# Kernel tuning notes

Measured on AMD Instinct MI355X. Metric: run time of the kernel, lower is better.

## Reference

```python
import jax, jax.numpy as jnp
import numpy as np

LEAK = 0.2          # LeakyReLU negative slope
NEG = -9e15         # mask fill value from the original module
N, FIN, FOUT = 8192, 256, 128


def setup_inputs() -> dict:
    key = jax.random.key(0)
    k1, k2, k3, k4 = jax.random.split(key, 4)
    x = jax.random.normal(k1, (N, FIN), dtype=jnp.float32)
    # dense 0/1 adjacency mask, p(edge) ~= 0.5
    adj = jax.random.randint(k2, (N, N), 0, 2, dtype=jnp.int32)
    # xavier_uniform with gain sqrt(2)
    gW = np.sqrt(2.0) * np.sqrt(6.0 / (FIN + FOUT))
    W = jax.random.uniform(k3, (FIN, FOUT), dtype=jnp.float32, minval=-gW, maxval=gW)
    ga = np.sqrt(2.0) * np.sqrt(6.0 / (FOUT + 1))
    a = jax.random.uniform(k4, (FOUT, 1), dtype=jnp.float32, minval=-ga, maxval=ga)
    return {"x": x, "adj": adj, "W": W, "a": a}


def reference(x, adj, W, a):
    # h = X W                                     [N, FOUT]
    h = x @ W
    # alpha_j = a . h_j  -- the original's h.repeat(N,1) @ a reduces to this,
    # since every row block of the repeat is identical.
    alpha = jnp.squeeze(h @ a, axis=-1)           # [N]
    e = jax.nn.leaky_relu(alpha, LEAK)            # [N]
    # e_ij depends only on column j; broadcast across rows, then mask.
    scores = jnp.where(adj > 0, e[None, :], NEG)  # [N, N]
    attention = jax.nn.softmax(scores, axis=1)    # [N, N]
    # dropout: eval mode (training=False) -> identity
    h_prime = attention @ h                       # [N, FOUT]
    return h_prime
```

## Files before the change

### kernel.cpp

```cpp
#include <hip/hip_runtime.h>
#include <hip/hip_bf16.h>

#define NN 8192
#define FIN 256
#define FOUT 128
#define KSPLIT 2
#define KHALF (NN / KSPLIT)

typedef __attribute__((ext_vector_type(8))) short short8;
typedef __attribute__((ext_vector_type(4))) float f32x4;
typedef unsigned short u16;

__device__ inline u16 bf16r(float v) {
  return __builtin_bit_cast(u16, __float2bfloat16(v));
}

__global__ __launch_bounds__(256) void k_prep(const float* __restrict__ x,
                                              const float* __restrict__ W,
                                              const float* __restrict__ a,
                                              float* __restrict__ wexp,
                                              u16* __restrict__ gT) {
  __shared__ float xs[32 * 256];
  __shared__ float ap[4][16];
  __shared__ float wsh[32];
  __shared__ u16 gsh[32][132];
  const int t = threadIdx.x;
  const int r0 = blockIdx.x * 32;

  const float4* xg = (const float4*)(x + (size_t)r0 * FIN);
  float4* xs4 = (float4*)xs;
#pragma unroll
  for (int p = 0; p < 8; ++p) xs4[p * 256 + t] = xg[p * 256 + t];
  __syncthreads();

  const int f = t & 127;
  const int half = t >> 7;
  float acc[16];
#pragma unroll
  for (int i = 0; i < 16; ++i) acc[i] = 0.f;

  const float4* xsr = (const float4*)(xs + half * 16 * 256);
  for (int k4 = 0; k4 < 64; ++k4) {
    float w0 = W[(k4 * 4 + 0) * FOUT + f];
    float w1 = W[(k4 * 4 + 1) * FOUT + f];
    float w2 = W[(k4 * 4 + 2) * FOUT + f];
    float w3 = W[(k4 * 4 + 3) * FOUT + f];
#pragma unroll
    for (int i = 0; i < 16; ++i) {
      float4 xv = xsr[i * 64 + k4];
      acc[i] = fmaf(xv.x, w0, acc[i]);
      acc[i] = fmaf(xv.y, w1, acc[i]);
      acc[i] = fmaf(xv.z, w2, acc[i]);
      acc[i] = fmaf(xv.w, w3, acc[i]);
    }
  }

  const float af = a[f];
  float part[16];
#pragma unroll
  for (int i = 0; i < 16; ++i) part[i] = acc[i] * af;
#pragma unroll
  for (int i = 0; i < 16; ++i) {
#pragma unroll
    for (int off = 32; off >= 1; off >>= 1) part[i] += __shfl_xor(part[i], off);
  }
  const int wvid = t >> 6;
  if ((t & 63) == 0) {
#pragma unroll
    for (int i = 0; i < 16; ++i) ap[wvid][i] = part[i];
  }
  __syncthreads();
  if (t < 32) {
    int i = t & 15, hh = t >> 4;
    float alpha = ap[hh * 2][i] + ap[hh * 2 + 1][i];
    float ee = alpha > 0.f ? alpha : 0.2f * alpha;
    float wv = __expf(fminf(ee, 80.f));
    wsh[t] = wv;
    wexp[r0 + t] = wv;
  }
  __syncthreads();

#pragma unroll
  for (int i = 0; i < 16; ++i) {
    int row = half * 16 + i;
    gsh[row][f] = bf16r(acc[i] * wsh[row]);
  }
  __syncthreads();

  const int ff = t >> 1;
  const int jc = (t & 1) * 16;
  u16* dst = gT + (size_t)ff * NN + r0 + jc;
#pragma unroll
  for (int q = 0; q < 4; ++q) {
    ushort4 v;
    v.x = gsh[jc + q * 4 + 0][ff];
    v.y = gsh[jc + q * 4 + 1][ff];
    v.z = gsh[jc + q * 4 + 2][ff];
    v.w = gsh[jc + q * 4 + 3][ff];
    *(ushort4*)(dst + q * 4) = v;
  }
}

__global__ __launch_bounds__(512, 4) void k_gemm(const int* __restrict__ adj,
                                                 const u16* __restrict__ gT,
                                                 const float* __restrict__ w,
                                                 float* __restrict__ numer,
                                                 float* __restrict__ denom) {
  __shared__ u16 Ash[2][32 * 64];
  __shared__ u16 Bsh[2][128 * 64];
  __shared__ float denom_sh[32];

  const int t = threadIdx.x;
  const int lane = t & 63;
  const int wvid = t >> 6;
  const int wr = wvid >> 2;
  const int wc = wvid & 3;
  const int r0 = blockIdx.x * 32;
  const int ks = blockIdx.y;
  const size_t kbase = (size_t)ks * KHALF;

  const int ar = t >> 4;
  const int ako = (t & 15) * 4;
  const int* adjrow = adj + (size_t)(r0 + ar) * NN + kbase + ako;
  const float* wp = w + kbase + ako;
  const int bfr = t >> 3;
  const int bck = (t & 7) * 8;
  const u16* gTb = gT + kbase + bck;

  f32x4 acc0 = {0.f, 0.f, 0.f, 0.f};
  f32x4 acc1 = {0.f, 0.f, 0.f, 0.f};
  float dpart = 0.f;

  int4 av;
  float4 wq;
  short8 bb0, bb1;

  auto LOAD = [&](int kt) {
    av = *(const int4*)(adjrow + kt * 64);
    wq = *(const float4*)(wp + kt * 64);
    const u16* gp = gTb + (size_t)bfr * NN + kt * 64;
    bb0 = *(const short8*)gp;
    bb1 = *(const short8*)(gp + (size_t)64 * NN);
  };
  auto STORE = [&](int buf) {
    dpart += (av.x ? wq.x : 0.f) + (av.y ? wq.y : 0.f) +
             (av.z ? wq.z : 0.f) + (av.w ? wq.w : 0.f);
    ushort4 a4;
    a4.x = av.x ? (u16)0x3F80 : (u16)0;
    a4.y = av.y ? (u16)0x3F80 : (u16)0;
    a4.z = av.z ? (u16)0x3F80 : (u16)0;
    a4.w = av.w ? (u16)0x3F80 : (u16)0;
    int abyte = ar * 128 + ((ako * 2) ^ ((ar & 7) << 4));
    *(ushort4*)((char*)&Ash[buf][0] + abyte) = a4;
    int bbyte = bfr * 128 + ((bck * 2) ^ ((bfr & 7) << 4));
    *(short8*)((char*)&Bsh[buf][0] + bbyte) = bb0;
    *(short8*)((char*)&Bsh[buf][0] + bbyte + 64 * 128) = bb1;
  };
  auto COMPUTE = [&](int buf) {
    const int swz = (lane & 7) << 4;
    const int arow = wr * 16 + (lane & 15);
    const int bcol = wc * 32 + (lane & 15);
#pragma unroll
    for (int kc = 0; kc < 2; ++kc) {
      int kbyte = kc * 64 + (lane >> 4) * 16;
      short8 afr = *(const short8*)((const char*)&Ash[buf][0] + arow * 128 + (kbyte ^ swz));
      short8 b0  = *(const short8*)((const char*)&Bsh[buf][0] + bcol * 128 + (kbyte ^ swz));
      short8 b1  = *(const short8*)((const char*)&Bsh[buf][0] + (bcol + 16) * 128 + (kbyte ^ swz));
      acc0 = __builtin_amdgcn_mfma_f32_16x16x32_bf16(afr, b0, acc0, 0, 0, 0);
      acc1 = __builtin_amdgcn_mfma_f32_16x16x32_bf16(afr, b1, acc1, 0, 0, 0);
    }
  };

  const int NT = KHALF / 64;
  LOAD(0);
  STORE(0);
  LOAD(1);
  __syncthreads();
  for (int kt = 0; kt < NT; ++kt) {
    int buf = kt & 1;
    if (kt + 1 < NT) STORE(buf ^ 1);
    if (kt + 2 < NT) LOAD(kt + 2);
    COMPUTE(buf);
    __syncthreads();
  }

  dpart += __shfl_xor(dpart, 1);
  dpart += __shfl_xor(dpart, 2);
  dpart += __shfl_xor(dpart, 4);
  dpart += __shfl_xor(dpart, 8);
  if ((t & 15) == 0) denom_sh[ar] = dpart;
  __syncthreads();

#pragma unroll
  for (int q = 0; q < 4; ++q) {
    int row = wr * 16 + (lane >> 4) * 4 + q;
    int col = wc * 32 + (lane & 15);
    float* np = numer + ((size_t)ks * NN + r0 + row) * FOUT + col;
    np[0] = acc0[q];
    np[16] = acc1[q];
  }
  if (t < 32) denom[(size_t)ks * NN + r0 + t] = denom_sh[t];
}

__global__ __launch_bounds__(256) void k_comb(const float* __restrict__ numer,
                                              const float* __restrict__ denom,
                                              float* __restrict__ out) {
  const int idx = blockIdx.x * 256 + threadIdx.x;
  const int row = idx >> 5;
  const int fc = (idx & 31) * 4;
  float4 n0 = *(const float4*)(numer + (size_t)row * FOUT + fc);
  float4 n1 = *(const float4*)(numer + (size_t)(NN + row) * FOUT + fc);
  float d = denom[row] + denom[NN + row];
  float inv = 1.0f / d;
  float4 o;
  o.x = (n0.x + n1.x) * inv;
  o.y = (n0.y + n1.y) * inv;
  o.z = (n0.z + n1.z) * inv;
  o.w = (n0.w + n1.w) * inv;
  *(float4*)(out + (size_t)row * FOUT + fc) = o;
}

extern "C" void kernel_launch(void* const* d_in, const int* in_sizes, int n_in,
                              void* d_out, int out_size, void* d_ws, size_t ws_size,
                              hipStream_t stream) {
  const float* x = (const float*)d_in[0];
  const int* adj = (const int*)d_in[1];
  const float* W = (const float*)d_in[2];
  const float* a = (const float*)d_in[3];
  float* out = (float*)d_out;

  char* ws = (char*)d_ws;
  float* wexp = (float*)ws;
  u16* gT = (u16*)(ws + 64 * 1024);
  float* numer = (float*)(ws + 4 * 1024 * 1024);
  float* denom = (float*)(ws + 12 * 1024 * 1024);

  hipLaunchKernelGGL(k_prep, dim3(NN / 32), dim3(256), 0, stream, x, W, a, wexp, gT);
  hipLaunchKernelGGL(k_gemm, dim3(NN / 32, KSPLIT), dim3(512), 0, stream, adj, gT, wexp,
                     numer, denom);
  hipLaunchKernelGGL(k_comb, dim3((NN * FOUT / 4) / 256), dim3(256), 0, stream, numer,
                     denom, out);
}
```

Measured before the change: 96.44 us.

## Deepen global prefetch to four register sets with manual barrier scheduling

Changes the k_gemm main loop from a distance-2 register prefetch to a rotating set of four register stages, so global loads run about four tiles ahead. LDS fragment reads are issued before a single barrier per iteration, with sched_barrier and explicit waitcnt, so MFMAs run after the barrier. The aim is to hide HBM latency on the adjacency and gT streams. The extra registers may lower occupancy, and the hand-placed waits and barriers put correctness at risk if the double-buffer reuse ordering is wrong.

```diff
diff --git a/kernel.cpp b/kernel.cpp
--- a/kernel.cpp
+++ b/kernel.cpp
@@ -125,64 +125,98 @@
   const float* wp = w + kbase + ako;
   const int bfr = t >> 3;
   const int bck = (t & 7) * 8;
-  const u16* gTb = gT + kbase + bck;
-
+  const u16* gTb = gT + kbase + (size_t)bfr * NN + bck;
+
+  struct Set {
+    int4 av;
+    float4 wq;
+    short8 bb0, bb1;
+  };
+  Set s0, s1, s2, s3;
   f32x4 acc0 = {0.f, 0.f, 0.f, 0.f};
   f32x4 acc1 = {0.f, 0.f, 0.f, 0.f};
   float dpart = 0.f;
 
-  int4 av;
-  float4 wq;
-  short8 bb0, bb1;
-
-  auto LOAD = [&](int kt) {
-    av = *(const int4*)(adjrow + kt * 64);
-    wq = *(const float4*)(wp + kt * 64);
-    const u16* gp = gTb + (size_t)bfr * NN + kt * 64;
-    bb0 = *(const short8*)gp;
-    bb1 = *(const short8*)(gp + (size_t)64 * NN);
-  };
-  auto STORE = [&](int buf) {
-    dpart += (av.x ? wq.x : 0.f) + (av.y ? wq.y : 0.f) +
-             (av.z ? wq.z : 0.f) + (av.w ? wq.w : 0.f);
+  const int abyte = ar * 128 + ((ako * 2) ^ ((ar & 7) << 4));
+  const int bbyte = bfr * 128 + ((bck * 2) ^ ((bfr & 7) << 4));
+  const int swz = (lane & 7) << 4;
+  const int arow = wr * 16 + (lane & 15);
+  const int bcol = wc * 32 + (lane & 15);
+  const int k0 = (lane >> 4) * 16;
+
+  auto LOAD = [&](Set& S, int T) {
+    S.av = *(const int4*)(adjrow + T * 64);
+    S.wq = *(const float4*)(wp + T * 64);
+    S.bb0 = *(const short8*)(gTb + T * 64);
+    S.bb1 = *(const short8*)(gTb + T * 64 + (size_t)64 * NN);
+  };
+  auto STORE = [&](Set& S, int buf) {
+    dpart += (S.av.x ? S.wq.x : 0.f) + (S.av.y ? S.wq.y : 0.f) +
+             (S.av.z ? S.wq.z : 0.f) + (S.av.w ? S.wq.w : 0.f);
     ushort4 a4;
-    a4.x = av.x ? (u16)0x3F80 : (u16)0;
-    a4.y = av.y ? (u16)0x3F80 : (u16)0;
-    a4.z = av.z ? (u16)0x3F80 : (u16)0;
-    a4.w = av.w ? (u16)0x3F80 : (u16)0;
-    int abyte = ar * 128 + ((ako * 2) ^ ((ar & 7) << 4));
+    a4.x = S.av.x ? (u16)0x3F80 : (u16)0;
+    a4.y = S.av.y ? (u16)0x3F80 : (u16)0;
+    a4.z = S.av.z ? (u16)0x3F80 : (u16)0;
+    a4.w = S.av.w ? (u16)0x3F80 : (u16)0;
     *(ushort4*)((char*)&Ash[buf][0] + abyte) = a4;
-    int bbyte = bfr * 128 + ((bck * 2) ^ ((bfr & 7) << 4));
-    *(short8*)((char*)&Bsh[buf][0] + bbyte) = bb0;
-    *(short8*)((char*)&Bsh[buf][0] + bbyte + 64 * 128) = bb1;
-  };
-  auto COMPUTE = [&](int buf) {
-    const int swz = (lane & 7) << 4;
-    const int arow = wr * 16 + (lane & 15);
-    const int bcol = wc * 32 + (lane & 15);
-#pragma unroll
-    for (int kc = 0; kc < 2; ++kc) {
-      int kbyte = kc * 64 + (lane >> 4) * 16;
-      short8 afr = *(const short8*)((const char*)&Ash[buf][0] + arow * 128 + (kbyte ^ swz));
-      short8 b0  = *(const short8*)((const char*)&Bsh[buf][0] + bcol * 128 + (kbyte ^ swz));
-      short8 b1  = *(const short8*)((const char*)&Bsh[buf][0] + (bcol + 16) * 128 + (kbyte ^ swz));
-      acc0 = __builtin_amdgcn_mfma_f32_16x16x32_bf16(afr, b0, acc0, 0, 0, 0);
-      acc1 = __builtin_amdgcn_mfma_f32_16x16x32_bf16(afr, b1, acc1, 0, 0, 0);
-    }
-  };
-
-  const int NT = KHALF / 64;
-  LOAD(0);
-  STORE(0);
-  LOAD(1);
-  __syncthreads();
-  for (int kt = 0; kt < NT; ++kt) {
-    int buf = kt & 1;
-    if (kt + 1 < NT) STORE(buf ^ 1);
-    if (kt + 2 < NT) LOAD(kt + 2);
-    COMPUTE(buf);
-    __syncthreads();
-  }
+    *(short8*)((char*)&Bsh[buf][0] + bbyte) = S.bb0;
+    *(short8*)((char*)&Bsh[buf][0] + bbyte + 64 * 128) = S.bb1;
+  };
+
+  short8 fa0, fb00, fb10, fa1, fb01, fb11;
+  auto READS = [&](int buf) {
+    const char* A = (const char*)&Ash[buf][0];
+    const char* B = (const char*)&Bsh[buf][0];
+    fa0 = *(const short8*)(A + arow * 128 + (k0 ^ swz));
+    fb00 = *(const short8*)(B + bcol * 128 + (k0 ^ swz));
+    fb10 = *(const short8*)(B + (bcol + 16) * 128 + (k0 ^ swz));
+    fa1 = *(const short8*)(A + arow * 128 + ((64 + k0) ^ swz));
+    fb01 = *(const short8*)(B + bcol * 128 + ((64 + k0) ^ swz));
+    fb11 = *(const short8*)(B + (bcol + 16) * 128 + ((64 + k0) ^ swz));
+  };
+  auto MFMAS = [&]() {
+    acc0 = __builtin_amdgcn_mfma_f32_16x16x32_bf16(fa0, fb00, acc0, 0, 0, 0);
+    acc1 = __builtin_amdgcn_mfma_f32_16x16x32_bf16(fa0, fb10, acc1, 0, 0, 0);
+    acc0 = __builtin_amdgcn_mfma_f32_16x16x32_bf16(fa1, fb01, acc0, 0, 0, 0);
+    acc1 = __builtin_amdgcn_mfma_f32_16x16x32_bf16(fa1, fb11, acc1, 0, 0, 0);
+  };
+
+#define BODY(J, SW, DOST, DOLD)                             \
+  do {                                                      \
+    if (DOST) STORE(SW, ((J) + 1) & 1);                     \
+    if (DOLD) LOAD(SW, (J) + 5);                            \
+    READS((J) & 1);                                         \
+    asm volatile("s_waitcnt lgkmcnt(0)" ::: "memory");      \
+    __builtin_amdgcn_s_barrier();                           \
+    __builtin_amdgcn_sched_barrier(0);                      \
+    MFMAS();                                                \
+  } while (0)
+
+  LOAD(s0, 0);
+  STORE(s0, 0);
+  LOAD(s1, 1);
+  LOAD(s2, 2);
+  LOAD(s3, 3);
+  LOAD(s0, 4);
+  asm volatile("s_waitcnt lgkmcnt(0)" ::: "memory");
+  __builtin_amdgcn_s_barrier();
+  __builtin_amdgcn_sched_barrier(0);
+
+  for (int jb = 0; jb < 56; jb += 4) {
+    BODY(jb + 0, s1, 1, 1);
+    BODY(jb + 1, s2, 1, 1);
+    BODY(jb + 2, s3, 1, 1);
+    BODY(jb + 3, s0, 1, 1);
+  }
+  BODY(56, s1, 1, 1);
+  BODY(57, s2, 1, 1);
+  BODY(58, s3, 1, 1);
+  BODY(59, s0, 1, 0);
+  BODY(60, s1, 1, 0);
+  BODY(61, s2, 1, 0);
+  BODY(62, s3, 1, 0);
+  BODY(63, s0, 0, 0);
+#undef BODY
 
   dpart += __shfl_xor(dpart, 1);
   dpart += __shfl_xor(dpart, 2);
```

Result: no change. 97.89 us (+1.5%).

## Replace LDS-staged GEMM with register-direct MFMA and split K four ways

Applied to the files above, without the earlier changes.

The adjacency-weighted GEMM no longer stages tiles in LDS. Each wave loads its adjacency fragment directly into MFMA operand layout with nontemporal loads, packs the 0/1 values into bf16 with an integer multiply, and reads gT B-fragments straight from global memory with double-buffered registers. K is split four ways instead of two, and the combine kernel sums four partials. This removes LDS stores, loads and block barriers. In exchange each wave rereads the full B panel from global/L2, uses more registers, and writes more partial output.

```diff
diff --git a/kernel.cpp b/kernel.cpp
--- a/kernel.cpp
+++ b/kernel.cpp
@@ -4,12 +4,16 @@
 #define NN 8192
 #define FIN 256
 #define FOUT 128
-#define KSPLIT 2
-#define KHALF (NN / KSPLIT)
+#define KSPLIT 4
+#define KCH (NN / KSPLIT)
+#define NT (KCH / 32)
 
 typedef __attribute__((ext_vector_type(8))) short short8;
 typedef __attribute__((ext_vector_type(4))) float f32x4;
+typedef __attribute__((ext_vector_type(4))) int i32x4;
+typedef __attribute__((ext_vector_type(4))) unsigned int u32x4;
 typedef unsigned short u16;
+typedef unsigned int u32;
 
 __device__ inline u16 bf16r(float v) {
   return __builtin_bit_cast(u16, __float2bfloat16(v));
@@ -101,105 +105,99 @@
   }
 }
 
-__global__ __launch_bounds__(512, 4) void k_gemm(const int* __restrict__ adj,
-                                                 const u16* __restrict__ gT,
-                                                 const float* __restrict__ w,
-                                                 float* __restrict__ numer,
-                                                 float* __restrict__ denom) {
-  __shared__ u16 Ash[2][32 * 64];
-  __shared__ u16 Bsh[2][128 * 64];
-  __shared__ float denom_sh[32];
-
+__global__ __launch_bounds__(256) void k_mm(const int* __restrict__ adj,
+                                            const u16* __restrict__ gT,
+                                            const float* __restrict__ wexp,
+                                            float* __restrict__ numer,
+                                            float* __restrict__ denom) {
   const int t = threadIdx.x;
   const int lane = t & 63;
-  const int wvid = t >> 6;
-  const int wr = wvid >> 2;
-  const int wc = wvid & 3;
-  const int r0 = blockIdx.x * 32;
+  const int wv = t >> 6;
+  const int i0 = blockIdx.x * 64 + wv * 16;
   const int ks = blockIdx.y;
-  const size_t kbase = (size_t)ks * KHALF;
-
-  const int ar = t >> 4;
-  const int ako = (t & 15) * 4;
-  const int* adjrow = adj + (size_t)(r0 + ar) * NN + kbase + ako;
-  const float* wp = w + kbase + ako;
-  const int bfr = t >> 3;
-  const int bck = (t & 7) * 8;
-  const u16* gTb = gT + kbase + bck;
-
-  f32x4 acc0 = {0.f, 0.f, 0.f, 0.f};
-  f32x4 acc1 = {0.f, 0.f, 0.f, 0.f};
+  const int kbase = ks * KCH;
+  const int r = lane & 15;
+  const int ksl = lane >> 4;
+
+  const int* ap = adj + (size_t)(i0 + r) * NN + kbase + ksl * 8;
+  const float* wp = wexp + kbase + ksl * 8;
+  const u16* gp = gT + (size_t)r * NN + kbase + ksl * 8;
+
+  f32x4 acc[8];
+#pragma unroll
+  for (int n = 0; n < 8; ++n) acc[n] = (f32x4){0.f, 0.f, 0.f, 0.f};
   float dpart = 0.f;
 
-  int4 av;
-  float4 wq;
-  short8 bb0, bb1;
-
-  auto LOAD = [&](int kt) {
-    av = *(const int4*)(adjrow + kt * 64);
-    wq = *(const float4*)(wp + kt * 64);
-    const u16* gp = gTb + (size_t)bfr * NN + kt * 64;
-    bb0 = *(const short8*)gp;
-    bb1 = *(const short8*)(gp + (size_t)64 * NN);
+  i32x4 avE0, avE1, avO0, avO1;
+  f32x4 wvE0, wvE1, wvO0, wvO1;
+  short8 fbE[8], fbO[8];
+
+  auto LDA = [&](int kt, i32x4& a0, i32x4& a1, f32x4& w0, f32x4& w1) {
+    const i32x4* p = (const i32x4*)(ap + kt * 32);
+    a0 = __builtin_nontemporal_load(p);
+    a1 = __builtin_nontemporal_load(p + 1);
+    const f32x4* q = (const f32x4*)(wp + kt * 32);
+    w0 = q[0];
+    w1 = q[1];
   };
-  auto STORE = [&](int buf) {
-    dpart += (av.x ? wq.x : 0.f) + (av.y ? wq.y : 0.f) +
-             (av.z ? wq.z : 0.f) + (av.w ? wq.w : 0.f);
-    ushort4 a4;
-    a4.x = av.x ? (u16)0x3F80 : (u16)0;
-    a4.y = av.y ? (u16)0x3F80 : (u16)0;
-    a4.z = av.z ? (u16)0x3F80 : (u16)0;
-    a4.w = av.w ? (u16)0x3F80 : (u16)0;
-    int abyte = ar * 128 + ((ako * 2) ^ ((ar & 7) << 4));
-    *(ushort4*)((char*)&Ash[buf][0] + abyte) = a4;
-    int bbyte = bfr * 128 + ((bck * 2) ^ ((bfr & 7) << 4));
-    *(short8*)((char*)&Bsh[buf][0] + bbyte) = bb0;
-    *(short8*)((char*)&Bsh[buf][0] + bbyte + 64 * 128) = bb1;
+  auto LDB = [&](int kt, short8* fb) {
+#pragma unroll
+    for (int n = 0; n < 8; ++n)
+      fb[n] = *(const short8*)(gp + (size_t)n * 16 * NN + kt * 32);
   };
-  auto COMPUTE = [&](int buf) {
-    const int swz = (lane & 7) << 4;
-    const int arow = wr * 16 + (lane & 15);
-    const int bcol = wc * 32 + (lane & 15);
-#pragma unroll
-    for (int kc = 0; kc < 2; ++kc) {
-      int kbyte = kc * 64 + (lane >> 4) * 16;
-      short8 afr = *(const short8*)((const char*)&Ash[buf][0] + arow * 128 + (kbyte ^ swz));
-      short8 b0  = *(const short8*)((const char*)&Bsh[buf][0] + bcol * 128 + (kbyte ^ swz));
-      short8 b1  = *(const short8*)((const char*)&Bsh[buf][0] + (bcol + 16) * 128 + (kbyte ^ swz));
-      acc0 = __builtin_amdgcn_mfma_f32_16x16x32_bf16(afr, b0, acc0, 0, 0, 0);
-      acc1 = __builtin_amdgcn_mfma_f32_16x16x32_bf16(afr, b1, acc1, 0, 0, 0);
+  auto STEP = [&](i32x4 a0, i32x4 a1, f32x4 w0, f32x4 w1, short8* fb) {
+    u32 p0 = ((u32)a0[0] + ((u32)a0[1] << 16)) * 0x3F80u;
+    u32 p1 = ((u32)a0[2] + ((u32)a0[3] << 16)) * 0x3F80u;
+    u32 p2 = ((u32)a1[0] + ((u32)a1[1] << 16)) * 0x3F80u;
+    u32 p3 = ((u32)a1[2] + ((u32)a1[3] << 16)) * 0x3F80u;
+    u32x4 pv = {p0, p1, p2, p3};
+    short8 fa = __builtin_bit_cast(short8, pv);
+    dpart += (a0[0] ? w0[0] : 0.f) + (a0[1] ? w0[1] : 0.f) +
+             (a0[2] ? w0[2] : 0.f) + (a0[3] ? w0[3] : 0.f) +
+             (a1[0] ? w1[0] : 0.f) + (a1[1] ? w1[1] : 0.f) +
+             (a1[2] ? w1[2] : 0.f) + (a1[3] ? w1[3] : 0.f);
+#pragma unroll
+    for (int n = 0; n < 8; ++n)
+      acc[n] = __builtin_amdgcn_mfma_f32_16x16x32_bf16(fa, fb[n], acc[n], 0, 0, 0);
+  };
+
+  LDA(0, avE0, avE1, wvE0, wvE1);
+  LDA(1, avO0, avO1, wvO0, wvO1);
+  LDB(0, fbE);
+
+#pragma unroll 1
+  for (int kt = 0; kt < NT; kt += 2) {
+    {
+      i32x4 a0 = avE0, a1 = avE1;
+      f32x4 w0 = wvE0, w1 = wvE1;
+      int ka = (kt + 2 < NT) ? kt + 2 : 0;
+      LDA(ka, avE0, avE1, wvE0, wvE1);
+      LDB(kt + 1, fbO);
+      STEP(a0, a1, w0, w1, fbE);
     }
-  };
-
-  const int NT = KHALF / 64;
-  LOAD(0);
-  STORE(0);
-  LOAD(1);
-  __syncthreads();
-  for (int kt = 0; kt < NT; ++kt) {
-    int buf = kt & 1;
-    if (kt + 1 < NT) STORE(buf ^ 1);
-    if (kt + 2 < NT) LOAD(kt + 2);
-    COMPUTE(buf);
-    __syncthreads();
-  }
-
-  dpart += __shfl_xor(dpart, 1);
-  dpart += __shfl_xor(dpart, 2);
-  dpart += __shfl_xor(dpart, 4);
-  dpart += __shfl_xor(dpart, 8);
-  if ((t & 15) == 0) denom_sh[ar] = dpart;
-  __syncthreads();
-
+    {
+      i32x4 a0 = avO0, a1 = avO1;
+      f32x4 w0 = wvO0, w1 = wvO1;
+      int ka = (kt + 3 < NT) ? kt + 3 : 0;
+      LDA(ka, avO0, avO1, wvO0, wvO1);
+      int kb = (kt + 2 < NT) ? kt + 2 : 0;
+      LDB(kb, fbE);
+      STEP(a0, a1, w0, w1, fbO);
+    }
+  }
+
+  dpart += __shfl_xor(dpart, 16);
+  dpart += __shfl_xor(dpart, 32);
+  if (lane < 16) denom[(size_t)ks * NN + i0 + lane] = dpart;
+
+  float* np = numer + ((size_t)ks * NN + i0) * FOUT;
 #pragma unroll
   for (int q = 0; q < 4; ++q) {
-    int row = wr * 16 + (lane >> 4) * 4 + q;
-    int col = wc * 32 + (lane & 15);
-    float* np = numer + ((size_t)ks * NN + r0 + row) * FOUT + col;
-    np[0] = acc0[q];
-    np[16] = acc1[q];
-  }
-  if (t < 32) denom[(size_t)ks * NN + r0 + t] = denom_sh[t];
+    int row = (lane >> 4) * 4 + q;
+#pragma unroll
+    for (int n = 0; n < 8; ++n)
+      np[(size_t)row * FOUT + n * 16 + (lane & 15)] = acc[n][q];
+  }
 }
 
 __global__ __launch_bounds__(256) void k_comb(const float* __restrict__ numer,
@@ -208,15 +206,23 @@
   const int idx = blockIdx.x * 256 + threadIdx.x;
   const int row = idx >> 5;
   const int fc = (idx & 31) * 4;
-  float4 n0 = *(const float4*)(numer + (size_t)row * FOUT + fc);
-  float4 n1 = *(const float4*)(numer + (size_t)(NN + row) * FOUT + fc);
-  float d = denom[row] + denom[NN + row];
+  float4 s = {0.f, 0.f, 0.f, 0.f};
+  float d = 0.f;
+#pragma unroll
+  for (int ks = 0; ks < KSPLIT; ++ks) {
+    float4 nv = *(const float4*)(numer + ((size_t)ks * NN + row) * FOUT + fc);
+    s.x += nv.x;
+    s.y += nv.y;
+    s.z += nv.z;
+    s.w += nv.w;
+    d += denom[(size_t)ks * NN + row];
+  }
   float inv = 1.0f / d;
   float4 o;
-  o.x = (n0.x + n1.x) * inv;
-  o.y = (n0.y + n1.y) * inv;
-  o.z = (n0.z + n1.z) * inv;
-  o.w = (n0.w + n1.w) * inv;
+  o.x = s.x * inv;
+  o.y = s.y * inv;
+  o.z = s.z * inv;
+  o.w = s.w * inv;
   *(float4*)(out + (size_t)row * FOUT + fc) = o;
 }
 
@@ -231,12 +237,12 @@
 
   char* ws = (char*)d_ws;
   float* wexp = (float*)ws;
-  u16* gT = (u16*)(ws + 64 * 1024);
-  float* numer = (float*)(ws + 4 * 1024 * 1024);
-  float* denom = (float*)(ws + 12 * 1024 * 1024);
+  u16* gT = (u16*)(ws + (size_t)65536);
+  float* numer = (float*)(ws + (size_t)65536 + 2097152);
+  float* denom = (float*)(ws + (size_t)65536 + 2097152 + 16777216);
 
   hipLaunchKernelGGL(k_prep, dim3(NN / 32), dim3(256), 0, stream, x, W, a, wexp, gT);
-  hipLaunchKernelGGL(k_gemm, dim3(NN / 32, KSPLIT), dim3(512), 0, stream, adj, gT, wexp,
+  hipLaunchKernelGGL(k_mm, dim3(NN / 64, KSPLIT), dim3(256), 0, stream, adj, gT, wexp,
                      numer, denom);
   hipLaunchKernelGGL(k_comb, dim3((NN * FOUT / 4) / 256), dim3(256), 0, stream, numer,
                      denom, out);
```

Result: slower. 203.6 us (+111.1%).
